# Kernel optimization log

Measured on AMD Instinct MI355X. Metric: run time of the kernel, lower is better.

Reference implementation:

```python
import jax, jax.numpy as jnp
import numpy as np

N_NODES = 40960
N_EDGES = 655360
IN_DIM = 128
HID = 128
HEADS = 4
CH = HID // HEADS  # per-head channels = 32
N_GRAPHS = 16
NEG_SLOPE = 0.2


def setup_inputs() -> dict:
    key = jax.random.key(0)
    ks = jax.random.split(key, 32)
    inp = {
        "x": jax.random.normal(ks[0], (N_NODES, IN_DIM), dtype=jnp.float32),
        "edge_index": jax.random.randint(ks[1], (2, N_EDGES), 0, N_NODES, dtype=jnp.int64),
        "batch_vec": jnp.sort(jax.random.randint(ks[2], (N_NODES,), 0, N_GRAPHS, dtype=jnp.int64)),
    }
    dims = [(IN_DIM, HID), (HID, HID), (HID, HID)]
    ki = 3
    for l, (din, dout) in enumerate(dims):
        s = 1.0 / np.sqrt(din)
        inp[f"Wl{l}"] = jax.random.normal(ks[ki + 0], (din, dout), dtype=jnp.float32) * s
        inp[f"bl{l}"] = jnp.zeros((dout,), dtype=jnp.float32)
        inp[f"Wr{l}"] = jax.random.normal(ks[ki + 1], (din, dout), dtype=jnp.float32) * s
        inp[f"br{l}"] = jnp.zeros((dout,), dtype=jnp.float32)
        inp[f"att{l}"] = jax.random.normal(ks[ki + 2], (HEADS, CH), dtype=jnp.float32) * (1.0 / np.sqrt(CH))
        inp[f"b{l}"] = jnp.zeros((dout,), dtype=jnp.float32)
        ki += 3
    return inp


def _gatv2_layer(x, src, dst, Wl, bl, Wr, br, att, bias):
    # GATv2Conv (PyG semantics, add_self_loops=True handled by caller's src/dst)
    n = x.shape[0]
    xl = (x @ Wl + bl).reshape(n, HEADS, CH)  # source transform
    xr = (x @ Wr + br).reshape(n, HEADS, CH)  # destination transform
    m = xl[src] + xr[dst]                      # [E, H, C]
    e = jnp.einsum("ehc,hc->eh", jax.nn.leaky_relu(m, NEG_SLOPE), att)  # [E, H]
    emax = jax.ops.segment_max(e, dst, num_segments=n)
    ex = jnp.exp(e - emax[dst])
    denom = jax.ops.segment_sum(ex, dst, num_segments=n)
    alpha = ex / denom[dst]                    # segment softmax over in-edges
    out = jax.ops.segment_sum(alpha[:, :, None] * xl[src], dst, num_segments=n)
    return out.reshape(n, HEADS * CH) + bias


def reference(x, edge_index, batch_vec,
              Wl0, bl0, Wr0, br0, att0, b0,
              Wl1, bl1, Wr1, br1, att1, b1,
              Wl2, bl2, Wr2, br2, att2, b2):
    n = x.shape[0]
    loops = jnp.arange(n, dtype=edge_index.dtype)
    src = jnp.concatenate([edge_index[0], loops])  # PyG default add_self_loops=True
    dst = jnp.concatenate([edge_index[1], loops])

    h = _gatv2_layer(x, src, dst, Wl0, bl0, Wr0, br0, att0, b0)
    h = jax.nn.relu(h)
    h = _gatv2_layer(h, src, dst, Wl1, bl1, Wr1, br1, att1, b1)
    h = jax.nn.relu(h)
    h = _gatv2_layer(h, src, dst, Wl2, bl2, Wr2, br2, att2, b2)

    # global_mean_pool over batch assignment
    sums = jax.ops.segment_sum(h, batch_vec, num_segments=N_GRAPHS)
    cnt = jax.ops.segment_sum(jnp.ones((n,), dtype=h.dtype), batch_vec, num_segments=N_GRAPHS)
    pooled = sums / jnp.maximum(cnt, 1.0)[:, None]
    return pooled, h
```

## Files before the change

### kernel.cpp

```cpp
#include <hip/hip_runtime.h>

#define NN 40960
#define NE 655360
#define ET (NE + NN)
#define D 128
#define NG 16
#define PL 16896

typedef unsigned int u32;
typedef unsigned short u16;
typedef long long i64;
typedef __attribute__((ext_vector_type(8))) short bf8v;
typedef __attribute__((ext_vector_type(4))) float f4v;

struct P18 { const void* p[18]; };

__device__ __forceinline__ float bf2f(u16 v){ return __uint_as_float(((u32)v)<<16); }
__device__ __forceinline__ u16 f2bf(float f){
  u32 u = __float_as_uint(f);
  return (u16)((u + 0x7FFFu + ((u>>16)&1u)) >> 16);
}
__device__ __forceinline__ int geti(const void* p, long long i, int f64, int bound){
  long long v = f64 ? ((const i64*)p)[i] : (long long)((const int*)p)[i];
  int x = (int)v;
  return (x < 0) ? 0 : ((x >= bound) ? bound-1 : x);
}
__device__ __forceinline__ void stf(void* p, long long i, float v, int isbf){
  if (isbf) ((u16*)p)[i] = f2bf(v); else ((float*)p)[i] = v;
}
__device__ __forceinline__ float rdf(const void* p, long long i, int isbf){
  return isbf ? bf2f(((const u16*)p)[i]) : ((const float*)p)[i];
}
__device__ __forceinline__ float4 ldb4(const u16* p){
  ushort4 u = *(const ushort4*)p;
  return make_float4(bf2f(u.x), bf2f(u.y), bf2f(u.z), bf2f(u.w));
}

__global__ void k_setup(const void* __restrict__ ei, const void* __restrict__ x,
                        int* __restrict__ flags, u32* __restrict__ cursor, float* __restrict__ pool,
                        u32* __restrict__ csr){
  int b = blockIdx.x;
  if (b == 0){
    __shared__ int nz, cnt;
    if (threadIdx.x == 0){ nz = 0; cnt = 0; }
    __syncthreads();
    if (((const int*)ei)[2*threadIdx.x + 1] != 0) atomicAdd(&nz, 1);
    if (threadIdx.x < 128){
      u16 v = ((const u16*)x)[2*threadIdx.x];
      int ex = (v >> 7) & 0xFF;
      if (ex >= 100 && ex <= 140) atomicAdd(&cnt, 1);
    }
    __syncthreads();
    if (threadIdx.x == 0){
      flags[0] = (nz == 0) ? 1 : 0;
      flags[1] = (cnt >= 64) ? 1 : 0;
    }
  } else if (b <= 160){
    cursor[(b-1)*256 + threadIdx.x] = 0u;
  } else if (b <= 168){
    int i = (b-161)*256 + threadIdx.x;
    if (i < NG*D) pool[i] = 0.f;
  } else {
    if (threadIdx.x < 16) csr[ET + threadIdx.x] = 0u;
  }
}

__global__ void k_prep(P18 ps, const void* __restrict__ x, u16* __restrict__ xb,
                       float* __restrict__ prm, const int* __restrict__ flags){
  int b = blockIdx.x;
  int isbf = flags[1];
  if (b >= 390){
    long long i = (long long)(b - 390)*256 + threadIdx.x;
    xb[i] = f2bf(rdf(x, i, isbf));
    return;
  }
  int l = b / 130;
  int i = (b % 130)*256 + threadIdx.x;
  const void* Wl  = ps.p[6*l+0];
  const void* bl  = ps.p[6*l+1];
  const void* Wr  = ps.p[6*l+2];
  const void* br  = ps.p[6*l+3];
  const void* att = ps.p[6*l+4];
  const void* bb  = ps.p[6*l+5];
  float* p = prm + (size_t)l*PL;
  if (i < 32768){
    int n = i >> 7, k = i & 127;
    float v = (n < 128) ? rdf(Wl, k*128 + n, isbf) : rdf(Wr, k*128 + (n - 128), isbf);
    ((u16*)p)[i] = f2bf(v);
    return;
  }
  float* fb = p + 16384;
  if (i < 33024){ int gc = i - 32768; fb[gc] = (gc < 128) ? rdf(bl, gc, isbf) : rdf(br, gc - 128, isbf); }
  else if (i < 33152) fb[256 + (i - 33024)] = rdf(att, i - 33024, isbf);
  else                fb[384 + (i - 33152)] = rdf(bb, i - 33152, isbf);
}

__global__ void k_hist(const void* __restrict__ ei, u32* __restrict__ cursor, const int* __restrict__ flags){
  int e = blockIdx.x*256 + threadIdx.x;
  if (e >= ET) return;
  int dd = (e < NE) ? geti(ei, (long long)NE + e, flags[0], NN) : e - NE;
  atomicAdd(&cursor[dd], 1u);
}

__global__ __launch_bounds__(256) void k_scanA(const u32* __restrict__ cursor, u32* __restrict__ psum){
  __shared__ u32 red[256];
  int t = threadIdx.x;
  red[t] = cursor[blockIdx.x*256 + t];
  __syncthreads();
  #pragma unroll
  for (int off = 128; off > 0; off >>= 1){
    if (t < off) red[t] += red[t + off];
    __syncthreads();
  }
  if (t == 0) psum[blockIdx.x] = red[0];
}

__global__ __launch_bounds__(256) void k_scanB(u32* __restrict__ psum, u32* __restrict__ offs,
                                               const void* __restrict__ batch, u32* __restrict__ bnd,
                                               const int* __restrict__ flags){
  __shared__ u32 sh[256];
  int t = threadIdx.x;
  sh[t] = (t < 160) ? psum[t] : 0u;
  __syncthreads();
  #pragma unroll
  for (int off = 1; off < 256; off <<= 1){
    u32 add = (t >= off) ? sh[t - off] : 0u;
    __syncthreads();
    sh[t] += add;
    __syncthreads();
  }
  if (t < 160) psum[t] = (t == 0) ? 0u : sh[t - 1];
  if (t == 160) offs[NN] = sh[159];
  if (t >= 192 && t <= 192 + NG){
    int g = t - 192;
    if (g == NG){ bnd[NG] = NN; }
    else {
      int f = flags[0];
      int lo = 0, hi = NN;
      while (lo < hi){
        int mid = (lo + hi) >> 1;
        if (geti(batch, mid, f, NG) < g) lo = mid + 1; else hi = mid;
      }
      bnd[g] = (u32)lo;
    }
  }
}

__global__ __launch_bounds__(256) void k_scanC(u32* __restrict__ cursor, u32* __restrict__ offs,
                                               const u32* __restrict__ psum){
  __shared__ u32 sh[256];
  int t = threadIdx.x;
  int gi = blockIdx.x*256 + t;
  u32 v = cursor[gi];
  sh[t] = v;
  __syncthreads();
  #pragma unroll
  for (int off = 1; off < 256; off <<= 1){
    u32 add = (t >= off) ? sh[t - off] : 0u;
    __syncthreads();
    sh[t] += add;
    __syncthreads();
  }
  u32 excl = ((t > 0) ? sh[t - 1] : 0u) + psum[blockIdx.x];
  offs[gi] = excl;
  cursor[gi] = excl;
}

__global__ void k_scatter(const void* __restrict__ ei, u32* __restrict__ cursor,
                          u32* __restrict__ csr, const int* __restrict__ flags){
  int e = blockIdx.x*256 + threadIdx.x;
  if (e >= ET) return;
  int f = flags[0];
  int s, dd;
  if (e < NE){ s = geti(ei, e, f, NN); dd = geti(ei, (long long)NE + e, f, NN); }
  else { s = dd = e - NE; }
  u32 pos = atomicAdd(&cursor[dd], 1u);
  csr[pos] = (u32)s * D;
}

__global__ __launch_bounds__(256) void k_gemm(const u16* __restrict__ Xb, const float* __restrict__ pr,
                                              u16* __restrict__ xl, u16* __restrict__ xr)
{
  int wv = threadIdx.x >> 6, lane = threadIdx.x & 63;
  int row0 = blockIdx.x*64 + wv*16;
  int rA = lane & 15, ks = lane >> 4;
  const u16* wt     = (const u16*)pr;
  const float* bias = pr + 16384;

  const u16* xp = Xb + (size_t)(row0 + rA)*D + ks*8;
  bf8v a0 = *(const bf8v*)(xp);
  bf8v a1 = *(const bf8v*)(xp + 32);
  bf8v a2 = *(const bf8v*)(xp + 64);
  bf8v a3 = *(const bf8v*)(xp + 96);

  int n0 = blockIdx.y*4;
  #pragma unroll
  for (int t = 0; t < 4; ++t, ++n0){
    int gc = n0*16 + rA;
    const u16* wp = wt + (size_t)gc*D + ks*8;
    bf8v b0 = *(const bf8v*)(wp);
    bf8v b1 = *(const bf8v*)(wp + 32);
    bf8v b2 = *(const bf8v*)(wp + 64);
    bf8v b3 = *(const bf8v*)(wp + 96);
    float bv = bias[gc];
    f4v acc = {bv, bv, bv, bv};
    acc = __builtin_amdgcn_mfma_f32_16x16x32_bf16(a0, b0, acc, 0, 0, 0);
    acc = __builtin_amdgcn_mfma_f32_16x16x32_bf16(a1, b1, acc, 0, 0, 0);
    acc = __builtin_amdgcn_mfma_f32_16x16x32_bf16(a2, b2, acc, 0, 0, 0);
    acc = __builtin_amdgcn_mfma_f32_16x16x32_bf16(a3, b3, acc, 0, 0, 0);
    u16* dst = (gc < 128) ? xl : xr;
    int cc = (gc < 128) ? gc : gc - 128;
    #pragma unroll
    for (int r = 0; r < 4; ++r)
      dst[(size_t)(row0 + ks*4 + r)*D + cc] = f2bf(acc[r]);
  }
}

__global__ __launch_bounds__(256) void k_node(const u16* __restrict__ xl, const u16* __restrict__ xr,
    const u32* __restrict__ offs, const u32* __restrict__ csr, const float* __restrict__ pr,
    u16* __restrict__ hb, float* __restrict__ hf, void* __restrict__ out,
    const int* __restrict__ flags, int last)
{
  int node = blockIdx.x*4 + (threadIdx.x >> 6);
  int lane = threadIdx.x & 63;
  int half = lane >> 5;
  int c = (lane & 31) * 4;
  const u16* xlc = xl + c;
  float4 xrv  = ldb4(xr + (size_t)node*D + c);
  float4 attv = *(const float4*)(pr + 16640 + c);
  u32 j0 = offs[node], j1 = offs[node + 1];

  float mx = -1e30f, ssum = 0.f;
  float4 acc = make_float4(0.f, 0.f, 0.f, 0.f);

  u32 j = j0 + half;
  u32 o0 = csr[j], o1 = csr[j+2];
  float4 g0 = ldb4(xlc + o0);
  float4 g1 = ldb4(xlc + o1);
  u32 o2 = csr[j+4], o3 = csr[j+6];

  for (; j < j1; j += 4){
    float4 n0 = ldb4(xlc + o2);
    float4 n1 = ldb4(xlc + o3);
    u32 t0 = csr[j+8], t1 = csr[j+10];

    {
      float m, p;
      m = g0.x + xrv.x; p = fmaxf(m, 0.2f*m) * attv.x;
      m = g0.y + xrv.y; p = fmaf(fmaxf(m, 0.2f*m), attv.y, p);
      m = g0.z + xrv.z; p = fmaf(fmaxf(m, 0.2f*m), attv.z, p);
      m = g0.w + xrv.w; p = fmaf(fmaxf(m, 0.2f*m), attv.w, p);
      p += __shfl_xor(p, 1, 64);
      p += __shfl_xor(p, 2, 64);
      p += __shfl_xor(p, 4, 64);
      if (p > mx + 8.f){
        float eo = __expf(mx - p);
        ssum  *= eo;
        acc.x *= eo; acc.y *= eo; acc.z *= eo; acc.w *= eo;
        mx = p;
      }
      float en = __expf(p - mx);
      ssum += en;
      acc.x = fmaf(en, g0.x, acc.x);
      acc.y = fmaf(en, g0.y, acc.y);
      acc.z = fmaf(en, g0.z, acc.z);
      acc.w = fmaf(en, g0.w, acc.w);
    }
    if (j + 2 < j1){
      float m, p;
      m = g1.x + xrv.x; p = fmaxf(m, 0.2f*m) * attv.x;
      m = g1.y + xrv.y; p = fmaf(fmaxf(m, 0.2f*m), attv.y, p);
      m = g1.z + xrv.z; p = fmaf(fmaxf(m, 0.2f*m), attv.z, p);
      m = g1.w + xrv.w; p = fmaf(fmaxf(m, 0.2f*m), attv.w, p);
      p += __shfl_xor(p, 1, 64);
      p += __shfl_xor(p, 2, 64);
      p += __shfl_xor(p, 4, 64);
      if (p > mx + 8.f){
        float eo = __expf(mx - p);
        ssum  *= eo;
        acc.x *= eo; acc.y *= eo; acc.z *= eo; acc.w *= eo;
        mx = p;
      }
      float en = __expf(p - mx);
      ssum += en;
      acc.x = fmaf(en, g1.x, acc.x);
      acc.y = fmaf(en, g1.y, acc.y);
      acc.z = fmaf(en, g1.z, acc.z);
      acc.w = fmaf(en, g1.w, acc.w);
    }
    g0 = n0; g1 = n1; o2 = t0; o3 = t1;
  }

  float mo = __shfl_xor(mx, 32, 64);
  float so = __shfl_xor(ssum, 32, 64);
  float ax = __shfl_xor(acc.x, 32, 64);
  float ay = __shfl_xor(acc.y, 32, 64);
  float az = __shfl_xor(acc.z, 32, 64);
  float aw = __shfl_xor(acc.w, 32, 64);
  float n  = fmaxf(mx, mo);
  float e0 = __expf(mx - n), e1 = __expf(mo - n);
  ssum  = ssum*e0 + so*e1;
  acc.x = acc.x*e0 + ax*e1;
  acc.y = acc.y*e0 + ay*e1;
  acc.z = acc.z*e0 + az*e1;
  acc.w = acc.w*e0 + aw*e1;

  if (half == 0){
    float inv = 1.0f / fmaxf(ssum, 1e-30f);
    float4 bv = *(const float4*)(pr + 16768 + c);
    float4 v = make_float4(acc.x*inv + bv.x, acc.y*inv + bv.y,
                           acc.z*inv + bv.z, acc.w*inv + bv.w);
    if (!last){
      v.x = fmaxf(v.x, 0.f); v.y = fmaxf(v.y, 0.f);
      v.z = fmaxf(v.z, 0.f); v.w = fmaxf(v.w, 0.f);
      ushort4 o = make_ushort4(f2bf(v.x), f2bf(v.y), f2bf(v.z), f2bf(v.w));
      *(ushort4*)(hb + (size_t)node*D + c) = o;
    } else {
      *(float4*)(hf + (size_t)node*D + c) = v;
      int isbf = flags[1];
      long long o = (long long)NG*D + (long long)node*D + c;
      stf(out, o+0, v.x, isbf); stf(out, o+1, v.y, isbf);
      stf(out, o+2, v.z, isbf); stf(out, o+3, v.w, isbf);
    }
  }
}

__global__ __launch_bounds__(256) void k_pool1(const float* __restrict__ h, const u32* __restrict__ bnd,
                                               float* __restrict__ pool){
  __shared__ float red[256];
  int g = blockIdx.x >> 4, sl = blockIdx.x & 15;
  int ch = threadIdx.x & 127, ro = threadIdx.x >> 7;
  u32 b0 = bnd[g], b1 = bnd[g + 1];
  float acc = 0.f;
  for (u32 r = b0 + sl*2 + ro; r < b1; r += 32) acc += h[(size_t)r*D + ch];
  red[threadIdx.x] = acc;
  __syncthreads();
  if (threadIdx.x < 128)
    unsafeAtomicAdd(&pool[g*D + ch], red[threadIdx.x] + red[threadIdx.x + 128]);
}

__global__ void k_pool2(const float* __restrict__ pool, const u32* __restrict__ bnd,
                        void* __restrict__ out, const int* __restrict__ flags){
  int i = blockIdx.x*256 + threadIdx.x;
  if (i >= NG*D) return;
  int g = i >> 7;
  float c = (float)(bnd[g + 1] - bnd[g]);
  stf(out, i, pool[i] / fmaxf(c, 1.f), flags[1]);
}

extern "C" void kernel_launch(void* const* d_in, const int* in_sizes, int n_in,
                              void* d_out, int out_size, void* d_ws, size_t ws_size,
                              hipStream_t stream) {
  const void* x     = d_in[0];
  const void* ei    = d_in[1];
  const void* batch = d_in[2];

  const long long nf = (long long)NN*D + 3*PL + NG*D;
  const long long nh = (long long)NN*D*3;
  const long long nu = (NN + 1) + NN + (ET + 16) + (NG + 1) + 2 + 160;
  if (ws_size < (size_t)nf*4 + (size_t)nh*2 + (size_t)nu*4 + 256) return;

  float* ws    = (float*)d_ws;
  float* xf    = ws;
  u16*  xb    = (u16*)(xf + (size_t)NN*D);
  u16*  xl    = xb + (size_t)NN*D;
  u16*  xr    = xl + (size_t)NN*D;
  float* prm   = (float*)(xr + (size_t)NN*D);
  float* pool  = prm + 3*PL;
  u32*  offs   = (u32*)(pool + NG*D);
  u32*  cursor = offs + (NN + 1);
  u32*  csr    = cursor + NN;
  u32*  bnd    = csr + (ET + 16);
  u32*  psum   = bnd + (NG + 1);
  int*  flags  = (int*)(psum + 160);

  k_setup<<<170, 256, 0, stream>>>(ei, x, flags, cursor, pool, csr);
  P18 ps;
  for (int i = 0; i < 18; ++i) ps.p[i] = d_in[3 + i];
  k_prep<<<390 + (NN*D)/256, 256, 0, stream>>>(ps, x, xb, prm, flags);

  k_hist<<<ET/256, 256, 0, stream>>>(ei, cursor, flags);
  k_scanA<<<160, 256, 0, stream>>>(cursor, psum);
  k_scanB<<<1, 256, 0, stream>>>(psum, offs, batch, bnd, flags);
  k_scanC<<<160, 256, 0, stream>>>(cursor, offs, psum);
  k_scatter<<<ET/256, 256, 0, stream>>>(ei, cursor, csr, flags);

  for (int l = 0; l < 3; ++l){
    const float* p = prm + (size_t)l*PL;
    k_gemm<<<dim3(NN/64, 4), 256, 0, stream>>>(xb, p, xl, xr);
    k_node<<<NN/4, 256, 0, stream>>>(xl, xr, offs, csr, p, xb, xf, d_out, flags, l == 2);
  }
  k_pool1<<<NG*16, 256, 0, stream>>>(xf, bnd, pool);
  k_pool2<<<8, 256, 0, stream>>>(pool, bnd, d_out, flags);
}
```

Baseline: 320.4 us.

## Replicate CSR degree counters and compress CSR source indices to 16-bit

Histogram and scatter atomics now go to one of eight counter copies, chosen by edge index, so fewer atomics collide on the same address. The scan kernels turn the copies into per-copy offsets. CSR entries now hold 16-bit source node ids, valid because NN is below 65536, and the node kernel shifts them into row offsets, halving index traffic in the aggregation loops. In exchange, the counter array is eight times larger, so there is more setup zeroing and more scan memory traffic, and the order of edges within each destination changes.

```diff
diff --git a/kernel.cpp b/kernel.cpp
--- a/kernel.cpp
+++ b/kernel.cpp
@@ -6,6 +6,7 @@
 #define D 128
 #define NG 16
 #define PL 16896
+#define NREP 8
 
 typedef unsigned int u32;
 typedef unsigned short u16;
@@ -38,7 +39,7 @@
 
 __global__ void k_setup(const void* __restrict__ ei, const void* __restrict__ x,
                         int* __restrict__ flags, u32* __restrict__ cursor, float* __restrict__ pool,
-                        u32* __restrict__ csr){
+                        u16* __restrict__ csr){
   int b = blockIdx.x;
   if (b == 0){
     __shared__ int nz, cnt;
@@ -55,13 +56,13 @@
       flags[0] = (nz == 0) ? 1 : 0;
       flags[1] = (cnt >= 64) ? 1 : 0;
     }
-  } else if (b <= 160){
+  } else if (b <= 1280){
     cursor[(b-1)*256 + threadIdx.x] = 0u;
-  } else if (b <= 168){
-    int i = (b-161)*256 + threadIdx.x;
+  } else if (b <= 1288){
+    int i = (b-1281)*256 + threadIdx.x;
     if (i < NG*D) pool[i] = 0.f;
   } else {
-    if (threadIdx.x < 16) csr[ET + threadIdx.x] = 0u;
+    if (threadIdx.x < 16) csr[ET + threadIdx.x] = 0;
   }
 }
 
@@ -99,13 +100,23 @@
   int e = blockIdx.x*256 + threadIdx.x;
   if (e >= ET) return;
   int dd = (e < NE) ? geti(ei, (long long)NE + e, flags[0], NN) : e - NE;
-  atomicAdd(&cursor[dd], 1u);
-}
-
-__global__ __launch_bounds__(256) void k_scanA(const u32* __restrict__ cursor, u32* __restrict__ psum){
+  atomicAdd(&cursor[(e & (NREP-1))*NN + dd], 1u);
+}
+
+__global__ __launch_bounds__(256) void k_scanA(u32* __restrict__ cursor, u32* __restrict__ tot,
+                                               u32* __restrict__ psum){
   __shared__ u32 red[256];
   int t = threadIdx.x;
-  red[t] = cursor[blockIdx.x*256 + t];
+  int dd = blockIdx.x*256 + t;
+  u32 run = 0;
+  #pragma unroll
+  for (int r = 0; r < NREP; ++r){
+    u32 v = cursor[r*NN + dd];
+    cursor[r*NN + dd] = run;
+    run += v;
+  }
+  tot[dd] = run;
+  red[t] = run;
   __syncthreads();
   #pragma unroll
   for (int off = 128; off > 0; off >>= 1){
@@ -147,11 +158,11 @@
 }
 
 __global__ __launch_bounds__(256) void k_scanC(u32* __restrict__ cursor, u32* __restrict__ offs,
-                                               const u32* __restrict__ psum){
+                                               const u32* __restrict__ tot, const u32* __restrict__ psum){
   __shared__ u32 sh[256];
   int t = threadIdx.x;
-  int gi = blockIdx.x*256 + t;
-  u32 v = cursor[gi];
+  int dd = blockIdx.x*256 + t;
+  u32 v = tot[dd];
   sh[t] = v;
   __syncthreads();
   #pragma unroll
@@ -162,20 +173,22 @@
     __syncthreads();
   }
   u32 excl = ((t > 0) ? sh[t - 1] : 0u) + psum[blockIdx.x];
-  offs[gi] = excl;
-  cursor[gi] = excl;
+  offs[dd] = excl;
+  #pragma unroll
+  for (int r = 0; r < NREP; ++r)
+    cursor[r*NN + dd] += excl;
 }
 
 __global__ void k_scatter(const void* __restrict__ ei, u32* __restrict__ cursor,
-                          u32* __restrict__ csr, const int* __restrict__ flags){
+                          u16* __restrict__ csr, const int* __restrict__ flags){
   int e = blockIdx.x*256 + threadIdx.x;
   if (e >= ET) return;
   int f = flags[0];
   int s, dd;
   if (e < NE){ s = geti(ei, e, f, NN); dd = geti(ei, (long long)NE + e, f, NN); }
   else { s = dd = e - NE; }
-  u32 pos = atomicAdd(&cursor[dd], 1u);
-  csr[pos] = (u32)s * D;
+  u32 pos = atomicAdd(&cursor[(e & (NREP-1))*NN + dd], 1u);
+  csr[pos] = (u16)s;
 }
 
 __global__ __launch_bounds__(256) void k_gemm(const u16* __restrict__ Xb, const float* __restrict__ pr,
@@ -217,7 +230,7 @@
 }
 
 __global__ __launch_bounds__(256) void k_node(const u16* __restrict__ xl, const u16* __restrict__ xr,
-    const u32* __restrict__ offs, const u32* __restrict__ csr, const float* __restrict__ pr,
+    const u32* __restrict__ offs, const u16* __restrict__ csr, const float* __restrict__ pr,
     u16* __restrict__ hb, float* __restrict__ hf, void* __restrict__ out,
     const int* __restrict__ flags, int last)
 {
@@ -234,15 +247,15 @@
   float4 acc = make_float4(0.f, 0.f, 0.f, 0.f);
 
   u32 j = j0 + half;
-  u32 o0 = csr[j], o1 = csr[j+2];
+  u32 o0 = ((u32)csr[j]) << 7, o1 = ((u32)csr[j+2]) << 7;
   float4 g0 = ldb4(xlc + o0);
   float4 g1 = ldb4(xlc + o1);
-  u32 o2 = csr[j+4], o3 = csr[j+6];
+  u32 o2 = ((u32)csr[j+4]) << 7, o3 = ((u32)csr[j+6]) << 7;
 
   for (; j < j1; j += 4){
     float4 n0 = ldb4(xlc + o2);
     float4 n1 = ldb4(xlc + o3);
-    u32 t0 = csr[j+8], t1 = csr[j+10];
+    u32 t0 = ((u32)csr[j+8]) << 7, t1 = ((u32)csr[j+10]) << 7;
 
     {
       float m, p;
@@ -357,8 +370,9 @@
 
   const long long nf = (long long)NN*D + 3*PL + NG*D;
   const long long nh = (long long)NN*D*3;
-  const long long nu = (NN + 1) + NN + (ET + 16) + (NG + 1) + 2 + 160;
-  if (ws_size < (size_t)nf*4 + (size_t)nh*2 + (size_t)nu*4 + 256) return;
+  const long long nu = (NN + 1) + (long long)NREP*NN + NN + (NG + 1) + 160 + 2;
+  const long long nc = ET + 16;
+  if (ws_size < (size_t)nf*4 + (size_t)nh*2 + (size_t)nu*4 + (size_t)nc*2 + 256) return;
 
   float* ws    = (float*)d_ws;
   float* xf    = ws;
@@ -369,20 +383,21 @@
   float* pool  = prm + 3*PL;
   u32*  offs   = (u32*)(pool + NG*D);
   u32*  cursor = offs + (NN + 1);
-  u32*  csr    = cursor + NN;
-  u32*  bnd    = csr + (ET + 16);
+  u32*  tot    = cursor + (size_t)NREP*NN;
+  u32*  bnd    = tot + NN;
   u32*  psum   = bnd + (NG + 1);
   int*  flags  = (int*)(psum + 160);
-
-  k_setup<<<170, 256, 0, stream>>>(ei, x, flags, cursor, pool, csr);
+  u16*  csr    = (u16*)(flags + 2);
+
+  k_setup<<<1290, 256, 0, stream>>>(ei, x, flags, cursor, pool, csr);
   P18 ps;
   for (int i = 0; i < 18; ++i) ps.p[i] = d_in[3 + i];
   k_prep<<<390 + (NN*D)/256, 256, 0, stream>>>(ps, x, xb, prm, flags);
 
   k_hist<<<ET/256, 256, 0, stream>>>(ei, cursor, flags);
-  k_scanA<<<160, 256, 0, stream>>>(cursor, psum);
+  k_scanA<<<160, 256, 0, stream>>>(cursor, tot, psum);
   k_scanB<<<1, 256, 0, stream>>>(psum, offs, batch, bnd, flags);
-  k_scanC<<<160, 256, 0, stream>>>(cursor, offs, psum);
+  k_scanC<<<160, 256, 0, stream>>>(cursor, offs, tot, psum);
   k_scatter<<<ET/256, 256, 0, stream>>>(ei, cursor, csr, flags);
 
   for (int l = 0; l < 3; ++l){
```

Result: faster. 313.8 us (-2.1%).
